# Kernel tuning notes

Measured on AMD Instinct MI355X. Metric: run time of the kernel, lower is better.

Reference implementation:

```python
import jax, jax.numpy as jnp
import numpy as np

B, S, A, K = 32768, 8, 20, 4   # batch, hand size, max_actions, max cards per action
E, H, D = 64, 4, 16            # card embed dim, heads, head dim


def setup_inputs() -> dict:
    key = jax.random.key(0)
    ks = jax.random.split(key, 16)
    def w(k, shape, scale=0.1):
        return jax.random.normal(k, shape, jnp.float32) * scale
    emb = w(ks[0], (54, E)).at[0].set(0.0)  # padding_idx=0 row zeroed
    return dict(
        hand_cards=jax.random.randint(ks[1], (B, S), 0, 54),
        game_state=jax.random.normal(ks[2], (B, 12), jnp.float32),
        hand_size=jax.random.randint(ks[3], (B,), 1, 9),
        action_card_indices=jax.random.randint(ks[4], (A, K), 0, 54),
        action_card_counts=jax.random.randint(ks[5], (A,), 0, K + 1),
        num_valid_actions=20,
        emb=emb,
        in_proj_w=w(ks[6], (3 * E, E)), in_proj_b=jnp.zeros((3 * E,), jnp.float32),
        out_w=w(ks[7], (E, E)), out_b=jnp.zeros((E,), jnp.float32),
        g1_w=w(ks[8], (64, 12)), g1_b=jnp.zeros((64,), jnp.float32),
        g2_w=w(ks[9], (32, 64)), g2_b=jnp.zeros((32,), jnp.float32),
        c1_w=w(ks[10], (128, 96)), c1_b=jnp.zeros((128,), jnp.float32),
        c2_w=w(ks[11], (128, 128)), c2_b=jnp.zeros((128,), jnp.float32),
        s1_w=w(ks[12], (64, 192)), s1_b=jnp.zeros((64,), jnp.float32),
        s2_w=w(ks[13], (32, 64)), s2_b=jnp.zeros((32,), jnp.float32),
        s3_w=w(ks[14], (1, 32)), s3_b=jnp.zeros((1,), jnp.float32),
    )


def reference(hand_cards, game_state, hand_size, action_card_indices,
              action_card_counts, num_valid_actions, emb,
              in_proj_w, in_proj_b, out_w, out_b,
              g1_w, g1_b, g2_w, g2_b, c1_w, c1_b, c2_w, c2_b,
              s1_w, s1_b, s2_w, s2_b, s3_w, s3_b):
    # --- hand embedding + self-attention over the 8-card hand ---
    x = emb[hand_cards]                                   # [B,S,E]
    mask = hand_cards != 0                                # key_padding_mask (True = real card)
    qkv = jnp.einsum('bse,fe->bsf', x, in_proj_w) + in_proj_b
    q, k, v = jnp.split(qkv, 3, axis=-1)
    qh = q.reshape(B, S, H, D); kh = k.reshape(B, S, H, D); vh = v.reshape(B, S, H, D)
    scores = jnp.einsum('bqhd,bkhd->bhqk', qh, kh) / jnp.float32(np.sqrt(D))
    scores = jnp.where(mask[:, None, None, :], scores, jnp.float32(-1e9))
    attn = jax.nn.softmax(scores, axis=-1)
    ah = jnp.einsum('bhqk,bkhd->bqhd', attn, vh).reshape(B, S, E)
    attended = ah @ out_w.T + out_b                       # [B,S,E]
    # mean over true hand length (clamped to >=1, as in torch code)
    hand_len = jnp.maximum(hand_size, 1).astype(jnp.float32)[:, None]
    hand_ctx = attended.sum(axis=1) / hand_len            # [B,E]
    # --- game state + combined context MLPs ---
    g = jax.nn.relu(game_state @ g1_w.T + g1_b)
    g = jax.nn.relu(g @ g2_w.T + g2_b)                    # [B,32]
    ctx = jnp.concatenate([hand_ctx, g], axis=-1)         # [B,96]
    ctx = jax.nn.relu(ctx @ c1_w.T + c1_b)
    ctx = jax.nn.relu(ctx @ c2_w.T + c2_b)                # [B,128]
    # --- per-action card repr: gather + masked mean (zeros if no cards) ---
    ae = emb[action_card_indices]                         # [A,K,E]
    amask = (jnp.arange(K)[None, :] < action_card_counts[:, None]).astype(jnp.float32)
    denom = jnp.maximum(action_card_counts, 1).astype(jnp.float32)[:, None]
    arep = (ae * amask[..., None]).sum(axis=1) / denom    # [A,E]
    # --- action scorer; concat(ctx, arep) split into two partial GEMMs ---
    h = jax.nn.relu(ctx @ s1_w[:, :128].T[..., :][None if False else slice(None)]  # noqa
                    if False else
                    (ctx @ s1_w[:, :128].T)[:, None, :] + (arep @ s1_w[:, 128:].T)[None, :, :] + s1_b)  # [B,A,64]
    h = jax.nn.relu(h @ s2_w.T + s2_b)                    # [B,A,32]
    score = (h @ s3_w.T + s3_b)[..., 0]                   # [B,A]
    valid = jnp.arange(A) < num_valid_actions
    return jnp.where(valid[None, :], score, jnp.float32(-1e8))
```

## Files before the change

kernel.cpp:

```cpp
#include <hip/hip_runtime.h>
#include <hip/hip_bf16.h>

#define NT 512
#define TB 16

typedef unsigned short u16;
typedef unsigned int u32;
typedef __attribute__((ext_vector_type(8))) short short8v;
typedef __attribute__((ext_vector_type(4))) float f32x4;

__device__ __forceinline__ float bf2f(u16 u) {
  union { u32 i; float f; } v; v.i = ((u32)u) << 16; return v.f;
}
__device__ __forceinline__ float2 up2(u32 p) {
  union { u32 i; float f; } a, b;
  a.i = p << 16; b.i = p & 0xffff0000u;
  return make_float2(a.f, b.f);
}
__device__ __forceinline__ u16 f2bf(float f) {
  union { float f; u32 i; } v; v.f = f;
  u32 r = v.i + 0x7fffu + ((v.i >> 16) & 1u);
  return (u16)(r >> 16);
}
__device__ __forceinline__ u32 pk2c(float a, float b) {
  u32 r;
  asm("v_cvt_pk_bf16_f32 %0, %1, %2" : "=v"(r) : "v"(a), "v"(b));
  return r;
}

__global__ void prep_kernel(const float* __restrict__ emb, const int* __restrict__ act_idx,
                            const int* __restrict__ act_cnt, const float* __restrict__ s1w,
                            const float* __restrict__ s1b, const float* __restrict__ ipw,
                            const float* __restrict__ s2w, const float* __restrict__ ow,
                            const float* __restrict__ g2w, const float* __restrict__ c1w,
                            const float* __restrict__ c2w, float* __restrict__ ws) {
  __shared__ float s_arep[20][64];
  int t = threadIdx.x;
  for (int o = t; o < 20 * 64; o += 256) {
    int a = o >> 6, k = o & 63;
    int cnt = act_cnt[a];
    float sum = 0.f;
#pragma unroll
    for (int j = 0; j < 4; ++j)
      if (j < cnt) sum += emb[act_idx[a * 4 + j] * 64 + k];
    s_arep[a][k] = sum / (float)(cnt > 1 ? cnt : 1);
  }
  __syncthreads();
  for (int o = t; o < 20 * 64; o += 256) {
    int a = o >> 6, f = o & 63;
    const float* wr = s1w + f * 192 + 128;
    float acc = s1b[f];
#pragma unroll 8
    for (int k = 0; k < 64; ++k) acc += s_arep[a][k] * wr[k];
    ws[o] = acc;
  }
  u16* wbf = (u16*)(ws + 1280);
  for (int o = t; o < 12288; o += 256) wbf[o] = f2bf(ipw[o]);
  for (int o = t; o < 2048;  o += 256) wbf[12288 + o] = f2bf(s2w[o]);
  for (int o = t; o < 4096;  o += 256) wbf[14336 + o] = f2bf(ow[o]);
  for (int o = t; o < 2048;  o += 256) wbf[18432 + o] = f2bf(g2w[o]);
  for (int o = t; o < 12288; o += 256) wbf[20480 + o] = f2bf(c1w[o]);
  for (int o = t; o < 16384; o += 256) wbf[32768 + o] = f2bf(c2w[o]);
  for (int o = t; o < 8192;  o += 256) {
    int f = o >> 7, k = o & 127;
    wbf[49152 + o] = f2bf(s1w[f * 192 + k]);
  }
}

__global__ __launch_bounds__(NT, 6) void policy_fused(
    const int* __restrict__ hand_cards, const float* __restrict__ game_state,
    const int* __restrict__ hand_size, const int* __restrict__ num_valid,
    const float* __restrict__ emb, const float* __restrict__ ipb,
    const float* __restrict__ ob, const float* __restrict__ g1w,
    const float* __restrict__ g1b, const float* __restrict__ g2b,
    const float* __restrict__ c1b, const float* __restrict__ c2b,
    const float* __restrict__ s2b, const float* __restrict__ s3w,
    const float* __restrict__ s3b, const float* __restrict__ ws,
    float* __restrict__ out)
{
  __shared__ __align__(16) unsigned char s_raw[52544];
  u16*   s_x     = (u16*)s_raw;
  u16*   s_qkv   = (u16*)s_raw;
  u16*   s_hxbf  = (u16*)(s_raw + 0);
  u16*   s_g1bf  = (u16*)(s_raw + 2304);
  u16*   s_ctxin = (u16*)(s_raw + 4608);
  u16*   s_ctxbf = (u16*)(s_raw + 7936);
  u16*   s_ctx2bf= (u16*)(s_raw + 12288);
  u16*   s_hbf   = (u16*)s_raw;
  float* s_s1a   = (float*)(s_raw + 46080);
  int*   s_cards  = (int*)(s_raw + 51200);
  float* s_invlen = (float*)(s_raw + 51712);
  float* s_gs    = (float*)(s_raw + 51776);

  const float* ws_s1bp = ws;
  const u16* wbf    = (const u16*)(ws + 1280);
  const u16* wqkv   = wbf;
  const u16* s2wbf  = wbf + 12288;
  const u16* owbf   = wbf + 14336;
  const u16* g2wbf  = wbf + 18432;
  const u16* c1wbf  = wbf + 20480;
  const u16* c2wbf  = wbf + 32768;
  const u16* s1wbf  = wbf + 49152;

  const int t = threadIdx.x;
  const int base = blockIdx.x * TB;
  const int lw = t & 63, wv = t >> 6;
  const int kq = lw >> 4, rr = lw & 15;
  const int row0 = kq * 4;

  if (t < 128) s_cards[t] = hand_cards[base * 8 + t];
  if (t < TB) { int hs = hand_size[base + t]; s_invlen[t] = 1.0f / (float)(hs > 1 ? hs : 1); }
  if (t >= 128 && t < 128 + TB * 12) {
    int i = t - 128; s_gs[(i / 12) * 12 + (i % 12)] = game_state[(base + i / 12) * 12 + i % 12];
  }
  __syncthreads();

  {
    int es = t >> 2, k0 = (t & 3) * 16;
    const float* src = emb + s_cards[es] * 64 + k0;
    float4 v0 = *(const float4*)(src);
    float4 v1 = *(const float4*)(src + 4);
    float4 v2 = *(const float4*)(src + 8);
    float4 v3 = *(const float4*)(src + 12);
    uint4 pa = make_uint4(pk2c(v0.x,v0.y), pk2c(v0.z,v0.w), pk2c(v1.x,v1.y), pk2c(v1.z,v1.w));
    uint4 pb = make_uint4(pk2c(v2.x,v2.y), pk2c(v2.z,v2.w), pk2c(v3.x,v3.y), pk2c(v3.z,v3.w));
    *(uint4*)(s_x + es * 72 + k0) = pa;
    *(uint4*)(s_x + es * 72 + k0 + 8) = pb;
  }
  __syncthreads();

  {
    const int tok = wv * 16 + rr;
    short8v a0 = *(const short8v*)(s_x + tok * 72 + kq * 8);
    short8v a1 = *(const short8v*)(s_x + tok * 72 + 32 + kq * 8);
    __syncthreads();
    const int trow = wv * 16 + row0;
    for (int n = 0; n < 12; ++n) {
      const int f = n * 16 + rr;
      short8v b0 = *(const short8v*)(wqkv + f * 64 + kq * 8);
      short8v b1 = *(const short8v*)(wqkv + f * 64 + 32 + kq * 8);
      float bias = ipb[f];
      f32x4 acc = { bias, bias, bias, bias };
      acc = __builtin_amdgcn_mfma_f32_16x16x32_bf16(a0, b0, acc, 0, 0, 0);
      acc = __builtin_amdgcn_mfma_f32_16x16x32_bf16(a1, b1, acc, 0, 0, 0);
#pragma unroll
      for (int r = 0; r < 4; ++r)
        s_qkv[(trow + r) * 200 + f] = f2bf(acc[r]);
    }
  }
  __syncthreads();

  {
    int e = t >> 5, h = (t >> 3) & 3, q = t & 7;
    u16* qrow = s_qkv + (e * 8 + q) * 200 + h * 16;
    float qr[16];
    {
      uint4 ua = *(const uint4*)(qrow);
      uint4 ub = *(const uint4*)(qrow + 8);
      float2 f;
      f = up2(ua.x); qr[0]=f.x; qr[1]=f.y;  f = up2(ua.y); qr[2]=f.x; qr[3]=f.y;
      f = up2(ua.z); qr[4]=f.x; qr[5]=f.y;  f = up2(ua.w); qr[6]=f.x; qr[7]=f.y;
      f = up2(ub.x); qr[8]=f.x; qr[9]=f.y;  f = up2(ub.y); qr[10]=f.x; qr[11]=f.y;
      f = up2(ub.z); qr[12]=f.x; qr[13]=f.y; f = up2(ub.w); qr[14]=f.x; qr[15]=f.y;
    }
    float sc[8];
#pragma unroll
    for (int kk = 0; kk < 8; ++kk) {
      const u16* krow = s_qkv + (e * 8 + kk) * 200 + 64 + h * 16;
      uint4 ua = *(const uint4*)(krow);
      uint4 ub = *(const uint4*)(krow + 8);
      float a0 = 0.f;
      float2 f;
      f = up2(ua.x); a0 += qr[0]*f.x + qr[1]*f.y;
      f = up2(ua.y); a0 += qr[2]*f.x + qr[3]*f.y;
      f = up2(ua.z); a0 += qr[4]*f.x + qr[5]*f.y;
      f = up2(ua.w); a0 += qr[6]*f.x + qr[7]*f.y;
      f = up2(ub.x); a0 += qr[8]*f.x + qr[9]*f.y;
      f = up2(ub.y); a0 += qr[10]*f.x + qr[11]*f.y;
      f = up2(ub.z); a0 += qr[12]*f.x + qr[13]*f.y;
      f = up2(ub.w); a0 += qr[14]*f.x + qr[15]*f.y;
      sc[kk] = (s_cards[e * 8 + kk] != 0) ? a0 * 0.25f : -1e9f;
    }
    float m = sc[0];
#pragma unroll
    for (int kk = 1; kk < 8; ++kk) m = fmaxf(m, sc[kk]);
    float ssum = 0.f;
#pragma unroll
    for (int kk = 0; kk < 8; ++kk) { sc[kk] = __expf(sc[kk] - m); ssum += sc[kk]; }
    float inv = 1.f / ssum;
#pragma unroll
    for (int kk = 0; kk < 8; ++kk) sc[kk] *= inv;
    float acc[16];
#pragma unroll
    for (int d = 0; d < 16; ++d) acc[d] = 0.f;
#pragma unroll
    for (int kk = 0; kk < 8; ++kk) {
      const u16* vrow = s_qkv + (e * 8 + kk) * 200 + 128 + h * 16;
      uint4 ua = *(const uint4*)(vrow);
      uint4 ub = *(const uint4*)(vrow + 8);
      float2 f;
      f = up2(ua.x); acc[0] += sc[kk]*f.x; acc[1] += sc[kk]*f.y;
      f = up2(ua.y); acc[2] += sc[kk]*f.x; acc[3] += sc[kk]*f.y;
      f = up2(ua.z); acc[4] += sc[kk]*f.x; acc[5] += sc[kk]*f.y;
      f = up2(ua.w); acc[6] += sc[kk]*f.x; acc[7] += sc[kk]*f.y;
      f = up2(ub.x); acc[8] += sc[kk]*f.x; acc[9] += sc[kk]*f.y;
      f = up2(ub.y); acc[10] += sc[kk]*f.x; acc[11] += sc[kk]*f.y;
      f = up2(ub.z); acc[12] += sc[kk]*f.x; acc[13] += sc[kk]*f.y;
      f = up2(ub.w); acc[14] += sc[kk]*f.x; acc[15] += sc[kk]*f.y;
    }
    uint4 oa = make_uint4(pk2c(acc[0],acc[1]), pk2c(acc[2],acc[3]), pk2c(acc[4],acc[5]), pk2c(acc[6],acc[7]));
    uint4 oc = make_uint4(pk2c(acc[8],acc[9]), pk2c(acc[10],acc[11]), pk2c(acc[12],acc[13]), pk2c(acc[14],acc[15]));
    *(uint4*)(qrow) = oa;
    *(uint4*)(qrow + 8) = oc;
  }
  __syncthreads();

  {
    int e = t >> 5, k2 = (t & 31) * 2;
    float s0 = 0.f, s1 = 0.f;
#pragma unroll
    for (int q = 0; q < 8; ++q) {
      float2 f = up2(*(const u32*)(s_qkv + (e * 8 + q) * 200 + k2));
      s0 += f.x; s1 += f.y;
    }
    int e1 = t >> 6, f1 = t & 63;
    float ga = g1b[f1];
#pragma unroll
    for (int k = 0; k < 12; ++k) ga += s_gs[e1 * 12 + k] * g1w[f1 * 12 + k];
    int e2 = e1 + 8;
    float gb = g1b[f1];
#pragma unroll
    for (int k = 0; k < 12; ++k) gb += s_gs[e2 * 12 + k] * g1w[f1 * 12 + k];
    __syncthreads();
    *(u32*)(s_hxbf + e * 72 + k2) = pk2c(s0, s1);
    s_g1bf[e1 * 72 + f1] = f2bf(fmaxf(ga, 0.f));
    s_g1bf[e2 * 72 + f1] = f2bf(fmaxf(gb, 0.f));
  }
  __syncthreads();

  {
    if (wv < 4) {
      short8v a0 = *(const short8v*)(s_hxbf + rr * 72 + kq * 8);
      short8v a1 = *(const short8v*)(s_hxbf + rr * 72 + 32 + kq * 8);
      const int f = wv * 16 + rr;
      short8v b0 = *(const short8v*)(owbf + f * 64 + kq * 8);
      short8v b1 = *(const short8v*)(owbf + f * 64 + 32 + kq * 8);
      float bias = 8.f * ob[f];
      f32x4 acc = { bias, bias, bias, bias };
      acc = __builtin_amdgcn_mfma_f32_16x16x32_bf16(a0, b0, acc, 0, 0, 0);
      acc = __builtin_amdgcn_mfma_f32_16x16x32_bf16(a1, b1, acc, 0, 0, 0);
#pragma unroll
      for (int r = 0; r < 4; ++r) {
        int row = row0 + r;
        s_ctxin[row * 104 + f] = f2bf(acc[r] * s_invlen[row]);
      }
    } else if (wv < 6) {
      short8v g0 = *(const short8v*)(s_g1bf + rr * 72 + kq * 8);
      short8v g1v = *(const short8v*)(s_g1bf + rr * 72 + 32 + kq * 8);
      const int f2 = (wv - 4) * 16 + rr;
      short8v c0 = *(const short8v*)(g2wbf + f2 * 64 + kq * 8);
      short8v c1 = *(const short8v*)(g2wbf + f2 * 64 + 32 + kq * 8);
      float b2 = g2b[f2];
      f32x4 acc2 = { b2, b2, b2, b2 };
      acc2 = __builtin_amdgcn_mfma_f32_16x16x32_bf16(g0, c0, acc2, 0, 0, 0);
      acc2 = __builtin_amdgcn_mfma_f32_16x16x32_bf16(g1v, c1, acc2, 0, 0, 0);
#pragma unroll
      for (int r = 0; r < 4; ++r) {
        int row = row0 + r;
        s_ctxin[row * 104 + 64 + f2] = f2bf(fmaxf(acc2[r], 0.f));
      }
    }
  }
  __syncthreads();

  {
    short8v a0 = *(const short8v*)(s_ctxin + rr * 104 + kq * 8);
    short8v a1 = *(const short8v*)(s_ctxin + rr * 104 + 32 + kq * 8);
    short8v a2 = *(const short8v*)(s_ctxin + rr * 104 + 64 + kq * 8);
    const int f = wv * 16 + rr;
    short8v b0 = *(const short8v*)(c1wbf + f * 96 + kq * 8);
    short8v b1 = *(const short8v*)(c1wbf + f * 96 + 32 + kq * 8);
    short8v b2 = *(const short8v*)(c1wbf + f * 96 + 64 + kq * 8);
    float bias = c1b[f];
    f32x4 acc = { bias, bias, bias, bias };
    acc = __builtin_amdgcn_mfma_f32_16x16x32_bf16(a0, b0, acc, 0, 0, 0);
    acc = __builtin_amdgcn_mfma_f32_16x16x32_bf16(a1, b1, acc, 0, 0, 0);
    acc = __builtin_amdgcn_mfma_f32_16x16x32_bf16(a2, b2, acc, 0, 0, 0);
#pragma unroll
    for (int r = 0; r < 4; ++r) {
      int row = row0 + r;
      s_ctxbf[row * 136 + f] = f2bf(fmaxf(acc[r], 0.f));
    }
  }
  __syncthreads();

  {
    short8v a0 = *(const short8v*)(s_ctxbf + rr * 136 + kq * 8);
    short8v a1 = *(const short8v*)(s_ctxbf + rr * 136 + 32 + kq * 8);
    short8v a2 = *(const short8v*)(s_ctxbf + rr * 136 + 64 + kq * 8);
    short8v a3 = *(const short8v*)(s_ctxbf + rr * 136 + 96 + kq * 8);
    const int f = wv * 16 + rr;
    short8v b0 = *(const short8v*)(c2wbf + f * 128 + kq * 8);
    short8v b1 = *(const short8v*)(c2wbf + f * 128 + 32 + kq * 8);
    short8v b2 = *(const short8v*)(c2wbf + f * 128 + 64 + kq * 8);
    short8v b3 = *(const short8v*)(c2wbf + f * 128 + 96 + kq * 8);
    float bias = c2b[f];
    f32x4 acc = { bias, bias, bias, bias };
    acc = __builtin_amdgcn_mfma_f32_16x16x32_bf16(a0, b0, acc, 0, 0, 0);
    acc = __builtin_amdgcn_mfma_f32_16x16x32_bf16(a1, b1, acc, 0, 0, 0);
    acc = __builtin_amdgcn_mfma_f32_16x16x32_bf16(a2, b2, acc, 0, 0, 0);
    acc = __builtin_amdgcn_mfma_f32_16x16x32_bf16(a3, b3, acc, 0, 0, 0);
#pragma unroll
    for (int r = 0; r < 4; ++r) {
      int row = row0 + r;
      s_ctx2bf[row * 136 + f] = f2bf(fmaxf(acc[r], 0.f));
    }
  }
  __syncthreads();

  if (wv < 4) {
    short8v a0 = *(const short8v*)(s_ctx2bf + rr * 136 + kq * 8);
    short8v a1 = *(const short8v*)(s_ctx2bf + rr * 136 + 32 + kq * 8);
    short8v a2 = *(const short8v*)(s_ctx2bf + rr * 136 + 64 + kq * 8);
    short8v a3 = *(const short8v*)(s_ctx2bf + rr * 136 + 96 + kq * 8);
    const int f = wv * 16 + rr;
    short8v b0 = *(const short8v*)(s1wbf + f * 128 + kq * 8);
    short8v b1 = *(const short8v*)(s1wbf + f * 128 + 32 + kq * 8);
    short8v b2 = *(const short8v*)(s1wbf + f * 128 + 64 + kq * 8);
    short8v b3 = *(const short8v*)(s1wbf + f * 128 + 96 + kq * 8);
    f32x4 acc = { 0.f, 0.f, 0.f, 0.f };
    acc = __builtin_amdgcn_mfma_f32_16x16x32_bf16(a0, b0, acc, 0, 0, 0);
    acc = __builtin_amdgcn_mfma_f32_16x16x32_bf16(a1, b1, acc, 0, 0, 0);
    acc = __builtin_amdgcn_mfma_f32_16x16x32_bf16(a2, b2, acc, 0, 0, 0);
    acc = __builtin_amdgcn_mfma_f32_16x16x32_bf16(a3, b3, acc, 0, 0, 0);
#pragma unroll
    for (int r = 0; r < 4; ++r)
      s_s1a[(row0 + r) * 68 + f] = acc[r];
  }
  __syncthreads();

  for (int o = t; o < 320 * 32; o += NT) {
    int i = o >> 5, j = (o & 31) * 2;
    int e = i / 20, a = i - e * 20;
    float2 sv = *(const float2*)(s_s1a + e * 68 + j);
    float2 bv = *(const float2*)(ws_s1bp + a * 64 + j);
    float v0 = fmaxf(sv.x + bv.x, 0.f), v1 = fmaxf(sv.y + bv.y, 0.f);
    *(u32*)(s_hbf + i * 72 + j) = pk2c(v0, v1);
  }
  __syncthreads();

  {
    const int nv = num_valid[0];
    const float s3b0 = s3b[0];
    for (int mt = wv; mt < 20; mt += 8) {
      const int row = mt * 16 + rr;
      short8v a0 = *(const short8v*)(s_hbf + row * 72 + kq * 8);
      short8v a1 = *(const short8v*)(s_hbf + row * 72 + 32 + kq * 8);
      float part[4] = {0.f, 0.f, 0.f, 0.f};
#pragma unroll
      for (int ntile = 0; ntile < 2; ++ntile) {
        const int m = ntile * 16 + rr;
        short8v b0 = *(const short8v*)(s2wbf + m * 64 + kq * 8);
        short8v b1 = *(const short8v*)(s2wbf + m * 64 + 32 + kq * 8);
        float bias = s2b[m];
        f32x4 acc = { bias, bias, bias, bias };
        acc = __builtin_amdgcn_mfma_f32_16x16x32_bf16(a0, b0, acc, 0, 0, 0);
        acc = __builtin_amdgcn_mfma_f32_16x16x32_bf16(a1, b1, acc, 0, 0, 0);
        const float w3 = s3w[m];
#pragma unroll
        for (int r = 0; r < 4; ++r) part[r] += fmaxf(acc[r], 0.f) * w3;
      }
#pragma unroll
      for (int r = 0; r < 4; ++r) {
        part[r] += __shfl_xor(part[r], 1);
        part[r] += __shfl_xor(part[r], 2);
        part[r] += __shfl_xor(part[r], 4);
        part[r] += __shfl_xor(part[r], 8);
      }
      if (rr == 0) {
        const int i0 = mt * 16 + kq * 4;
#pragma unroll
        for (int r = 0; r < 4; ++r) {
          int i = i0 + r;
          int a = i - (i / 20) * 20;
          out[base * 20 + i] = (a < nv) ? (part[r] + s3b0) : -1e8f;
        }
      }
    }
  }
}

extern "C" void kernel_launch(void* const* d_in, const int* in_sizes, int n_in,
                              void* d_out, int out_size, void* d_ws, size_t ws_size,
                              hipStream_t stream) {
  (void)in_sizes; (void)n_in; (void)out_size; (void)ws_size;
  float* out = (float*)d_out;
  float* ws = (float*)d_ws;

  hipLaunchKernelGGL(prep_kernel, dim3(1), dim3(256), 0, stream,
                     (const float*)d_in[6], (const int*)d_in[3], (const int*)d_in[4],
                     (const float*)d_in[19], (const float*)d_in[20],
                     (const float*)d_in[7], (const float*)d_in[21],
                     (const float*)d_in[9], (const float*)d_in[13],
                     (const float*)d_in[15], (const float*)d_in[17], ws);
  hipLaunchKernelGGL(policy_fused, dim3(32768 / TB), dim3(NT), 0, stream,
                     (const int*)d_in[0],  (const float*)d_in[1], (const int*)d_in[2],
                     (const int*)d_in[5],
                     (const float*)d_in[6],  (const float*)d_in[8],
                     (const float*)d_in[10], (const float*)d_in[11],
                     (const float*)d_in[12], (const float*)d_in[14],
                     (const float*)d_in[16], (const float*)d_in[18],
                     (const float*)d_in[22], (const float*)d_in[23],
                     (const float*)d_in[24], ws, out);
}
```

Before: 126.5 us.

## Parallelize weight prep across blocks and fuse s1 bias-relu into MFMA operand load

The prep kernel moves from one block to 33: 32 blocks convert the weights to bf16 in parallel, and one block computes the per-action s1 projection. This removes a serial single-block prologue before the main kernel. In the main kernel, the bias+ReLU+bf16 pack of the scorer hidden layer is now done in registers while building the MFMA A operands. That drops a shared-memory staging pass and a barrier, at the cost of redundant float loads from LDS and from the global bias table per wave.

```diff
diff --git a/kernel.cpp b/kernel.cpp
--- a/kernel.cpp
+++ b/kernel.cpp
@@ -35,35 +35,39 @@
                             const float* __restrict__ g2w, const float* __restrict__ c1w,
                             const float* __restrict__ c2w, float* __restrict__ ws) {
   __shared__ float s_arep[20][64];
-  int t = threadIdx.x;
-  for (int o = t; o < 20 * 64; o += 256) {
-    int a = o >> 6, k = o & 63;
-    int cnt = act_cnt[a];
-    float sum = 0.f;
-#pragma unroll
-    for (int j = 0; j < 4; ++j)
-      if (j < cnt) sum += emb[act_idx[a * 4 + j] * 64 + k];
-    s_arep[a][k] = sum / (float)(cnt > 1 ? cnt : 1);
-  }
-  __syncthreads();
-  for (int o = t; o < 20 * 64; o += 256) {
-    int a = o >> 6, f = o & 63;
-    const float* wr = s1w + f * 192 + 128;
-    float acc = s1b[f];
+  const int b = blockIdx.x, t = threadIdx.x;
+  if (b < 32) {
+    const int tid = b * 256 + t;
+    u16* wbf = (u16*)(ws + 1280);
+    for (int o = tid; o < 12288; o += 8192) wbf[o] = f2bf(ipw[o]);
+    for (int o = tid; o < 2048;  o += 8192) wbf[12288 + o] = f2bf(s2w[o]);
+    for (int o = tid; o < 4096;  o += 8192) wbf[14336 + o] = f2bf(ow[o]);
+    for (int o = tid; o < 2048;  o += 8192) wbf[18432 + o] = f2bf(g2w[o]);
+    for (int o = tid; o < 12288; o += 8192) wbf[20480 + o] = f2bf(c1w[o]);
+    for (int o = tid; o < 16384; o += 8192) wbf[32768 + o] = f2bf(c2w[o]);
+    for (int o = tid; o < 8192;  o += 8192) {
+      int f = o >> 7, k = o & 127;
+      wbf[49152 + o] = f2bf(s1w[f * 192 + k]);
+    }
+  } else {
+    for (int o = t; o < 20 * 64; o += 256) {
+      int a = o >> 6, k = o & 63;
+      int cnt = act_cnt[a];
+      float sum = 0.f;
+#pragma unroll
+      for (int j = 0; j < 4; ++j)
+        if (j < cnt) sum += emb[act_idx[a * 4 + j] * 64 + k];
+      s_arep[a][k] = sum / (float)(cnt > 1 ? cnt : 1);
+    }
+    __syncthreads();
+    for (int o = t; o < 20 * 64; o += 256) {
+      int a = o >> 6, f = o & 63;
+      const float* wr = s1w + f * 192 + 128;
+      float acc = s1b[f];
 #pragma unroll 8
-    for (int k = 0; k < 64; ++k) acc += s_arep[a][k] * wr[k];
-    ws[o] = acc;
-  }
-  u16* wbf = (u16*)(ws + 1280);
-  for (int o = t; o < 12288; o += 256) wbf[o] = f2bf(ipw[o]);
-  for (int o = t; o < 2048;  o += 256) wbf[12288 + o] = f2bf(s2w[o]);
-  for (int o = t; o < 4096;  o += 256) wbf[14336 + o] = f2bf(ow[o]);
-  for (int o = t; o < 2048;  o += 256) wbf[18432 + o] = f2bf(g2w[o]);
-  for (int o = t; o < 12288; o += 256) wbf[20480 + o] = f2bf(c1w[o]);
-  for (int o = t; o < 16384; o += 256) wbf[32768 + o] = f2bf(c2w[o]);
-  for (int o = t; o < 8192;  o += 256) {
-    int f = o >> 7, k = o & 127;
-    wbf[49152 + o] = f2bf(s1w[f * 192 + k]);
+      for (int k = 0; k < 64; ++k) acc += s_arep[a][k] * wr[k];
+      ws[o] = acc;
+    }
   }
 }
 
@@ -86,7 +90,6 @@
   u16*   s_ctxin = (u16*)(s_raw + 4608);
   u16*   s_ctxbf = (u16*)(s_raw + 7936);
   u16*   s_ctx2bf= (u16*)(s_raw + 12288);
-  u16*   s_hbf   = (u16*)s_raw;
   float* s_s1a   = (float*)(s_raw + 46080);
   int*   s_cards  = (int*)(s_raw + 51200);
   float* s_invlen = (float*)(s_raw + 51712);
@@ -339,23 +342,34 @@
   }
   __syncthreads();
 
-  for (int o = t; o < 320 * 32; o += NT) {
-    int i = o >> 5, j = (o & 31) * 2;
-    int e = i / 20, a = i - e * 20;
-    float2 sv = *(const float2*)(s_s1a + e * 68 + j);
-    float2 bv = *(const float2*)(ws_s1bp + a * 64 + j);
-    float v0 = fmaxf(sv.x + bv.x, 0.f), v1 = fmaxf(sv.y + bv.y, 0.f);
-    *(u32*)(s_hbf + i * 72 + j) = pk2c(v0, v1);
-  }
-  __syncthreads();
-
   {
     const int nv = num_valid[0];
     const float s3b0 = s3b[0];
     for (int mt = wv; mt < 20; mt += 8) {
       const int row = mt * 16 + rr;
-      short8v a0 = *(const short8v*)(s_hbf + row * 72 + kq * 8);
-      short8v a1 = *(const short8v*)(s_hbf + row * 72 + 32 + kq * 8);
+      const int e = row / 20, a = row - e * 20;
+      const float* sa = s_s1a + e * 68;
+      const float* bp = ws_s1bp + a * 64;
+      float4 sA0 = *(const float4*)(sa + kq * 8);
+      float4 sA1 = *(const float4*)(sa + kq * 8 + 4);
+      float4 sB0 = *(const float4*)(sa + 32 + kq * 8);
+      float4 sB1 = *(const float4*)(sa + 32 + kq * 8 + 4);
+      float4 pA0 = *(const float4*)(bp + kq * 8);
+      float4 pA1 = *(const float4*)(bp + kq * 8 + 4);
+      float4 pB0 = *(const float4*)(bp + 32 + kq * 8);
+      float4 pB1 = *(const float4*)(bp + 32 + kq * 8 + 4);
+      union { short8v s8; uint4 u4; } A0, A1;
+      A0.u4 = make_uint4(
+        pk2c(fmaxf(sA0.x + pA0.x, 0.f), fmaxf(sA0.y + pA0.y, 0.f)),
+        pk2c(fmaxf(sA0.z + pA0.z, 0.f), fmaxf(sA0.w + pA0.w, 0.f)),
+        pk2c(fmaxf(sA1.x + pA1.x, 0.f), fmaxf(sA1.y + pA1.y, 0.f)),
+        pk2c(fmaxf(sA1.z + pA1.z, 0.f), fmaxf(sA1.w + pA1.w, 0.f)));
+      A1.u4 = make_uint4(
+        pk2c(fmaxf(sB0.x + pB0.x, 0.f), fmaxf(sB0.y + pB0.y, 0.f)),
+        pk2c(fmaxf(sB0.z + pB0.z, 0.f), fmaxf(sB0.w + pB0.w, 0.f)),
+        pk2c(fmaxf(sB1.x + pB1.x, 0.f), fmaxf(sB1.y + pB1.y, 0.f)),
+        pk2c(fmaxf(sB1.z + pB1.z, 0.f), fmaxf(sB1.w + pB1.w, 0.f)));
+      short8v a0 = A0.s8, a1 = A1.s8;
       float part[4] = {0.f, 0.f, 0.f, 0.f};
 #pragma unroll
       for (int ntile = 0; ntile < 2; ++ntile) {
@@ -382,8 +396,8 @@
 #pragma unroll
         for (int r = 0; r < 4; ++r) {
           int i = i0 + r;
-          int a = i - (i / 20) * 20;
-          out[base * 20 + i] = (a < nv) ? (part[r] + s3b0) : -1e8f;
+          int aa = i - (i / 20) * 20;
+          out[base * 20 + i] = (aa < nv) ? (part[r] + s3b0) : -1e8f;
         }
       }
     }
@@ -397,7 +411,7 @@
   float* out = (float*)d_out;
   float* ws = (float*)d_ws;
 
-  hipLaunchKernelGGL(prep_kernel, dim3(1), dim3(256), 0, stream,
+  hipLaunchKernelGGL(prep_kernel, dim3(33), dim3(256), 0, stream,
                      (const float*)d_in[6], (const int*)d_in[3], (const int*)d_in[4],
                      (const float*)d_in[19], (const float*)d_in[20],
                      (const float*)d_in[7], (const float*)d_in[21],
```

After: 123.2 us. 1.03x faster.
